# Kernel tuning notes

Measured on AMD Instinct MI355X. Metric: run time of the kernel, lower is better.

The kernel has to match this reference:

```python
import jax, jax.numpy as jnp
import numpy as np

K = 16          # neighboursnum
NEG_SLOPE = 0.01  # torch LeakyReLU default
EPS = 1e-5      # torch BatchNorm default


def _bn(x, gamma, beta, axes):
    # BatchNorm in training mode: biased batch stats over `axes`, channel dim = 1
    mu = x.mean(axes, keepdims=True)
    var = x.var(axes, keepdims=True)
    shape = [1] * x.ndim
    shape[1] = -1
    return (x - mu) / jnp.sqrt(var + EPS) * gamma.reshape(shape) + beta.reshape(shape)


def _lrelu(x):
    return jnp.where(x >= 0, x, NEG_SLOPE * x)


def setup_inputs() -> dict:
    key = jax.random.key(0)
    ks = jax.random.split(key, 9)
    B, D, N, O = 4, 64, 4096, 128
    s = 0.05
    return {
        "f_in": jax.random.normal(ks[0], (B, D, N), jnp.float32),
        "w_local": jax.random.normal(ks[1], (O, 2 * D + 1), jnp.float32) * s,
        "g_local": jnp.ones((O,), jnp.float32),
        "b_local": jnp.zeros((O,), jnp.float32),
        "w_sem": jax.random.normal(ks[2], (O, D), jnp.float32) * s,
        "g_sem": jnp.ones((O,), jnp.float32),
        "b_sem": jnp.zeros((O,), jnp.float32),
        "w_full": jax.random.normal(ks[3], (O, 2 * O), jnp.float32) * s,
        "g_full": jnp.ones((O,), jnp.float32),
        "b_full": jnp.zeros((O,), jnp.float32),
        "wq": jax.random.normal(ks[4], (D, D), jnp.float32) * s,
        "bq": jax.random.normal(ks[5], (D,), jnp.float32) * s,
        "wk": jax.random.normal(ks[6], (D, D), jnp.float32) * s,
        "bk": jax.random.normal(ks[7], (D,), jnp.float32) * s,
        "wv": jax.random.normal(ks[8], (D, D), jnp.float32) * s,
        "bv": jax.random.normal(jax.random.fold_in(key, 99), (D,), jnp.float32) * s,
    }


def reference(f_in, w_local, g_local, b_local, w_sem, g_sem, b_sem,
              w_full, g_full, b_full, wq, bq, wk, bk, wv, bv):
    B, D, N = f_in.shape
    # --- knn on feature space: pairwise negative squared distance, topk ---
    xx = jnp.sum(f_in * f_in, axis=1)                       # (B,N)
    inner = jnp.einsum('bdm,bdn->bmn', f_in, f_in)          # (B,N,N)
    pd = -xx[:, :, None] + 2.0 * inner - xx[:, None, :]     # -||xi-xj||^2
    idx = jax.lax.top_k(pd, K)[1]                           # (B,N,K) nearest
    # --- gather graph feature ---
    x_t = jnp.swapaxes(f_in, 1, 2)                          # (B,N,D)
    neigh = x_t[jnp.arange(B)[:, None, None], idx]          # (B,N,K,D)
    central = jnp.broadcast_to(x_t[:, :, None, :], neigh.shape)
    dist = jnp.linalg.norm(neigh - central, axis=3, keepdims=True)  # (B,N,K,1)
    feat = jnp.concatenate([central, neigh, dist], axis=3)  # (B,N,K,2D+1)
    feat = jnp.transpose(feat, (0, 3, 1, 2))                # (B,2D+1,N,K)
    # --- localConv (1x1 conv2d, no bias) + BN2d + LeakyReLU, max over K ---
    intra = _lrelu(_bn(jnp.einsum('oc,bcnk->bonk', w_local, feat),
                       g_local, b_local, (0, 2, 3)))
    intra = intra.max(axis=-1)                              # (B,O,N)
    # --- self-attention over points ---
    q = jnp.einsum('od,bdn->bon', wq, f_in) + bq[None, :, None]
    k = jnp.einsum('od,bdn->bon', wk, f_in) + bk[None, :, None]
    v = jnp.einsum('od,bdn->bon', wv, f_in) + bv[None, :, None]
    scores = jax.nn.softmax(
        jnp.einsum('bdm,bdn->bmn', q, k) / jnp.sqrt(jnp.float32(D)), axis=-1)
    fgt = jnp.einsum('bmn,bdn->bdm', scores, v)             # (B,D,N)
    # --- semConv (1x1 conv1d) + BN1d + LeakyReLU ---
    inter = _lrelu(_bn(jnp.einsum('od,bdn->bon', w_sem, fgt),
                       g_sem, b_sem, (0, 2)))               # (B,O,N)
    # --- fullConv on concat ---
    cat = jnp.concatenate([intra, inter], axis=1)           # (B,2O,N)
    out = _lrelu(_bn(jnp.einsum('oc,bcn->bon', w_full, cat),
                     g_full, b_full, (0, 2)))               # (B,O,N)
    return out
```

## Files before the change

### kernel.cpp

```cpp
#include <hip/hip_runtime.h>
#include <math.h>

constexpr int NB = 4;
constexpr int ND = 64;
constexpr int NNN = 4096;
constexpr int NO = 128;
constexpr int NK = 16;
constexpr float NEG = 0.01f;
constexpr float BN_EPS = 1e-5f;

typedef unsigned short u16;
typedef unsigned int u32;
typedef __attribute__((ext_vector_type(8))) short short8;
typedef __attribute__((ext_vector_type(4))) float floatx4;

constexpr int OFF_XX    = 0;
constexpr int OFF_IDX   = 16384;
constexpr int OFF_D2    = 278528;
constexpr int OFF_Q     = 540672;
constexpr int OFF_K     = 1589248;
constexpr int OFF_V     = 2637824;
constexpr int OFF_FGT   = 3686400;
constexpr int OFF_APRE  = 4734976;
constexpr int OFF_BPRE  = 6832128;
constexpr int OFF_IMAX  = 8929280;
constexpr int OFF_IMIN  = 11026432;
constexpr int OFF_ZSEM  = OFF_Q;
constexpr int OFF_ZFULL = OFF_V;
constexpr int OFF_STATS = 13123584;
constexpr int OFF_COEF  = 13124352;
constexpr int OFF_LINV  = 13125120;

__device__ __forceinline__ u16 f2b(float x) {
  u32 u = __builtin_bit_cast(u32, x);
  u += 0x7fffu + ((u >> 16) & 1u);
  return (u16)(u >> 16);
}
__device__ __forceinline__ float b2f(u16 h) {
  u32 u = (u32)h << 16;
  return __builtin_bit_cast(float, u);
}

template <int CTRL>
__device__ __forceinline__ float fmax_dpp(float v) {
  int b = __builtin_bit_cast(int, v);
  int s = __builtin_amdgcn_update_dpp(b, b, CTRL, 0xF, 0xF, false);
  return fmaxf(v, __builtin_bit_cast(float, s));
}
__device__ __forceinline__ void pairmax(float av, int ai, float bv, int bi, float& rv, int& ri) {
  bool tk = bv > av;
  rv = tk ? bv : av;
  ri = tk ? bi : ai;
}

__global__ void k_xx(const float* __restrict__ f, float* __restrict__ xx) {
  int gid = blockIdx.x * 256 + threadIdx.x;
  int b = gid >> 12, n = gid & 4095;
  const float* fb = f + b * ND * NNN + n;
  float s = 0.f;
#pragma unroll
  for (int d = 0; d < ND; ++d) { float v = fb[d * NNN]; s += v * v; }
  xx[gid] = s;
}

__global__ __launch_bounds__(256) void k_qkv(const float* __restrict__ f,
    const float* __restrict__ wq, const float* __restrict__ bq,
    const float* __restrict__ wk, const float* __restrict__ bk,
    const float* __restrict__ wv, const float* __restrict__ bv,
    u16* __restrict__ qb, u16* __restrict__ kb, u16* __restrict__ vb) {
  int sel = blockIdx.y;
  const float* W    = (sel == 0) ? wq : (sel == 1) ? wk : wv;
  const float* bias = (sel == 0) ? bq : (sel == 1) ? bk : bv;
  int t = threadIdx.x;
  int lane = t & 63;
  int og = __builtin_amdgcn_readfirstlane(t >> 6);
  int gcol = blockIdx.x * 64 + lane;
  int b = gcol >> 12, n = gcol & 4095;
  const float* fb = f + b * ND * NNN + n;
  float cv[64];
#pragma unroll
  for (int d = 0; d < ND; ++d) cv[d] = fb[d * NNN];
  float acc[16];
#pragma unroll 1
  for (int oi = 0; oi < 16; ++oi) {
    int o = og * 16 + oi;
    const float* wr = W + o * ND;
    float a = bias[o];
#pragma unroll
    for (int d = 0; d < ND; ++d) a += wr[d] * cv[d];
    acc[oi] = a;
  }
  if (sel == 2) {
#pragma unroll
    for (int oi = 0; oi < 16; ++oi)
      vb[(size_t)(b * ND + og * 16 + oi) * NNN + n] = f2b(acc[oi]);
  } else {
    short8 p0, p1;
#pragma unroll
    for (int oi = 0; oi < 8; ++oi) { p0[oi] = (short)f2b(acc[oi]); p1[oi] = (short)f2b(acc[8 + oi]); }
    u16* dst = (sel ? kb : qb) + (size_t)(b * NNN + n) * ND + og * 16;
    *(short8*)dst = p0;
    *(short8*)(dst + 8) = p1;
  }
}

__global__ __launch_bounds__(256, 4) void k_knn(const float* __restrict__ f, const float* __restrict__ xx,
                                                int* __restrict__ tidx, float* __restrict__ td2) {
  __shared__ __align__(16) float fm[ND * 8];
  __shared__ __align__(16) float sl[4 * 2048];
  int t = threadIdx.x;
  int lane = t & 63;
  int w = __builtin_amdgcn_readfirstlane(t >> 6);
  int b = blockIdx.x >> 9;
  int m0 = (blockIdx.x & 511) << 3;
  const float* fb = f + b * ND * NNN;
  { int e = t;       int d = e >> 3, r = e & 7; fm[e] = fb[d * NNN + m0 + r]; }
  { int e = t + 256; int d = e >> 3, r = e & 7; fm[e] = fb[d * NNN + m0 + r]; }
  __syncthreads();
  float lv[2][2];
  int   li[2][2];
#pragma unroll
  for (int h = 0; h < 2; ++h) {
    float acc[64];
#pragma unroll
    for (int i = 0; i < 64; ++i) acc[i] = 0.f;
    for (int d = 0; d < ND; ++d) {
      const float* frow = fb + d * NNN + h * 2048 + 4 * t;
      float4 v0 = *(const float4*)(frow);
      float4 v1 = *(const float4*)(frow + 1024);
      float4 r0 = *(const float4*)&fm[d * 8];
      float4 r1 = *(const float4*)&fm[d * 8 + 4];
      float va0[4] = {v0.x, v0.y, v0.z, v0.w};
      float va1[4] = {v1.x, v1.y, v1.z, v1.w};
      float rr[8]  = {r0.x, r0.y, r0.z, r0.w, r1.x, r1.y, r1.z, r1.w};
#pragma unroll
      for (int c2 = 0; c2 < 4; ++c2)
#pragma unroll
        for (int r = 0; r < 8; ++r) {
          acc[c2 * 8 + r]      += va0[c2] * rr[r];
          acc[32 + c2 * 8 + r] += va1[c2] * rr[r];
        }
    }
    {
      const float* xrow = xx + b * NNN + h * 2048 + 4 * t;
      float4 x0 = *(const float4*)(xrow);
      float4 x1 = *(const float4*)(xrow + 1024);
      float xa0[4] = {x0.x, x0.y, x0.z, x0.w};
      float xa1[4] = {x1.x, x1.y, x1.z, x1.w};
#pragma unroll
      for (int c2 = 0; c2 < 4; ++c2)
#pragma unroll
        for (int r = 0; r < 8; ++r) {
          acc[c2 * 8 + r]      = 2.f * acc[c2 * 8 + r]      - xa0[c2];
          acc[32 + c2 * 8 + r] = 2.f * acc[32 + c2 * 8 + r] - xa1[c2];
        }
    }
#pragma unroll
    for (int s = 0; s < 2; ++s) {
      __syncthreads();
#pragma unroll
      for (int r4 = 0; r4 < 4; ++r4) {
        int r = s * 4 + r4;
#pragma unroll
        for (int jj = 0; jj < 2; ++jj) {
          float4 w4;
          w4.x = acc[jj * 32 + 0 * 8 + r];
          w4.y = acc[jj * 32 + 1 * 8 + r];
          w4.z = acc[jj * 32 + 2 * 8 + r];
          w4.w = acc[jj * 32 + 3 * 8 + r];
          *(float4*)&sl[r4 * 2048 + jj * 1024 + 4 * t] = w4;
        }
      }
      __syncthreads();
      float vals[32];
#pragma unroll
      for (int i = 0; i < 32; ++i) vals[i] = sl[w * 2048 + i * 64 + lane];
      float gv[8]; int gi[8];
#pragma unroll
      for (int g = 0; g < 8; ++g) {
        float v0 = vals[g * 4]; int i0 = (g * 4) * 64 + lane;
#pragma unroll
        for (int k2 = 1; k2 < 4; ++k2)
          pairmax(v0, i0, vals[g * 4 + k2], (g * 4 + k2) * 64 + lane, v0, i0);
        gv[g] = v0; gi[g] = i0;
      }
      float t1v[4]; int t1i[4];
      float t2v[2]; int t2i[2];
      float lvv; int lii;
#pragma unroll
      for (int p = 0; p < 4; ++p) pairmax(gv[2 * p], gi[2 * p], gv[2 * p + 1], gi[2 * p + 1], t1v[p], t1i[p]);
#pragma unroll
      for (int q = 0; q < 2; ++q) pairmax(t1v[2 * q], t1i[2 * q], t1v[2 * q + 1], t1i[2 * q + 1], t2v[q], t2i[q]);
      pairmax(t2v[0], t2i[0], t2v[1], t2i[1], lvv, lii);
      float selv = 0.f; int seli = 0;
#pragma unroll 1
      for (int kx = 0; kx < NK; ++kx) {
        float W = lvv;
        W = fmax_dpp<0xB1>(W);
        W = fmax_dpp<0x4E>(W);
        W = fmax_dpp<0x124>(W);
        W = fmax_dpp<0x128>(W);
        W = fmaxf(W, __shfl_xor(W, 16));
        W = fmaxf(W, __shfl_xor(W, 32));
        unsigned long long mk = __ballot(lvv == W);
        int lw = (int)__ffsll(mk) - 1;
        int wcol = __builtin_amdgcn_readlane(lii, lw);
        if (lane == kx) { selv = W; seli = wcol; }
        int jw = wcol >> 6;
#pragma unroll
        for (int g = 0; g < 8; ++g)
          if (g == (jw >> 2)) {
#pragma unroll
            for (int k2 = 0; k2 < 4; ++k2)
              if (k2 == (jw & 3))
                vals[g * 4 + k2] = (lane == lw) ? -3.0e38f : vals[g * 4 + k2];
            float v0 = vals[g * 4]; int i0 = (g * 4) * 64 + lane;
#pragma unroll
            for (int k2 = 1; k2 < 4; ++k2)
              pairmax(v0, i0, vals[g * 4 + k2], (g * 4 + k2) * 64 + lane, v0, i0);
            gv[g] = v0; gi[g] = i0;
            int p = g >> 1;
            pairmax(gv[2 * p], gi[2 * p], gv[2 * p + 1], gi[2 * p + 1], t1v[p], t1i[p]);
            int q = p >> 1;
            pairmax(t1v[2 * q], t1i[2 * q], t1v[2 * q + 1], t1i[2 * q + 1], t2v[q], t2i[q]);
            pairmax(t2v[0], t2i[0], t2v[1], t2i[1], lvv, lii);
          }
      }
      lv[h][s] = selv; li[h][s] = h * 2048 + seli;
    }
  }
#pragma unroll
  for (int s = 0; s < 2; ++s) {
    int m = m0 + s * 4 + w;
    float xm = xx[b * NNN + m];
    float a   = lv[0][s]; int ai  = li[0][s];
    float bb2 = lv[1][s]; int bi2 = li[1][s];
    int cntB = 0, cntA = 0;
#pragma unroll
    for (int j = 0; j < 16; ++j) {
      float bj = __shfl(bb2, j);
      cntB += (bj > a) ? 1 : 0;
      float aj = __shfl(a, j);
      cntA += (aj >= bb2) ? 1 : 0;
    }
    if (lane < 16) {
      int base = (b * NNN + m) * NK;
      int rA = lane + cntB;
      int rB = lane + cntA;
      if (rA < NK) {
        float dd = xm - a;
        tidx[base + rA] = ai;
        td2[base + rA] = dd > 0.f ? dd : 0.f;
      }
      if (rB < NK) {
        float dd = xm - bb2;
        tidx[base + rB] = bi2;
        td2[base + rB] = dd > 0.f ? dd : 0.f;
      }
    }
  }
}

__global__ __launch_bounds__(256) void k_attn(const u16* __restrict__ qb,
                                              const u16* __restrict__ kb,
                                              const u16* __restrict__ vb,
                                              float* __restrict__ fgt,
                                              float* __restrict__ linv) {
  __shared__ __align__(16) u16 P[32 * 520];
  __shared__ float rsum[4][32];
  int t = threadIdx.x;
  int lane = t & 63;
  int w = __builtin_amdgcn_readfirstlane(t >> 6);
  int quad = lane >> 4;
  int l15 = lane & 15;
  int b = blockIdx.x >> 7;
  int m0 = (blockIdx.x & 127) << 5;
  const u16* qra = qb + (size_t)(b * NNN + m0 + l15) * ND + quad * 8;
  const u16* qrb = qb + (size_t)(b * NNN + m0 + 16 + l15) * ND + quad * 8;
  short8 qa0a = *(const short8*)(qra), qa1a = *(const short8*)(qra + 32);
  short8 qa0b = *(const short8*)(qrb), qa1b = *(const short8*)(qrb + 32);
  const u16* kbase = kb + (size_t)b * NNN * ND;
  const u16* vrow  = vb + (size_t)(b * ND + w * 16 + l15) * NNN;
  floatx4 c2a = {0.f, 0.f, 0.f, 0.f};
  floatx4 c2b = {0.f, 0.f, 0.f, 0.f};
  float rsa[4] = {0.f, 0.f, 0.f, 0.f};
  float rsb[4] = {0.f, 0.f, 0.f, 0.f};
#pragma unroll 1
  for (int it = 0; it < 8; ++it) {
    int nchunk = it * 512;
#pragma unroll 1
    for (int ct = 0; ct < 8; ++ct) {
      int cc0 = (w * 8 + ct) * 16;
      const u16* krow = kbase + (size_t)(nchunk + cc0 + l15) * ND + quad * 8;
      short8 kf0 = *(const short8*)(krow);
      short8 kf1 = *(const short8*)(krow + 32);
      floatx4 acca = {0.f, 0.f, 0.f, 0.f};
      acca = __builtin_amdgcn_mfma_f32_16x16x32_bf16(qa0a, kf0, acca, 0, 0, 0);
      acca = __builtin_amdgcn_mfma_f32_16x16x32_bf16(qa1a, kf1, acca, 0, 0, 0);
      floatx4 accb = {0.f, 0.f, 0.f, 0.f};
      accb = __builtin_amdgcn_mfma_f32_16x16x32_bf16(qa0b, kf0, accb, 0, 0, 0);
      accb = __builtin_amdgcn_mfma_f32_16x16x32_bf16(qa1b, kf1, accb, 0, 0, 0);
      int ccol = cc0 + l15;
#pragma unroll
      for (int r = 0; r < 4; ++r) {
        float ea = __expf(acca[r] * 0.125f);
        rsa[r] += ea;
        P[(quad * 4 + r) * 520 + ccol] = f2b(ea);
        float eb = __expf(accb[r] * 0.125f);
        rsb[r] += eb;
        P[(16 + quad * 4 + r) * 520 + ccol] = f2b(eb);
      }
    }
    __syncthreads();
    const u16* vp = vrow + nchunk + quad * 8;
#pragma unroll
    for (int kk = 0; kk < 16; ++kk) {
      short8 b2 = *(const short8*)(vp + kk * 32);
      short8 a2a = *(const short8*)&P[l15 * 520 + kk * 32 + quad * 8];
      short8 a2b = *(const short8*)&P[(16 + l15) * 520 + kk * 32 + quad * 8];
      c2a = __builtin_amdgcn_mfma_f32_16x16x32_bf16(a2a, b2, c2a, 0, 0, 0);
      c2b = __builtin_amdgcn_mfma_f32_16x16x32_bf16(a2b, b2, c2b, 0, 0, 0);
    }
    __syncthreads();
  }
#pragma unroll
  for (int r = 0; r < 4; ++r) {
    float va = rsa[r];
    va += __shfl_xor(va, 1); va += __shfl_xor(va, 2);
    va += __shfl_xor(va, 4); va += __shfl_xor(va, 8);
    rsa[r] = va;
    float vb2 = rsb[r];
    vb2 += __shfl_xor(vb2, 1); vb2 += __shfl_xor(vb2, 2);
    vb2 += __shfl_xor(vb2, 4); vb2 += __shfl_xor(vb2, 8);
    rsb[r] = vb2;
  }
  if (l15 == 0) {
#pragma unroll
    for (int r = 0; r < 4; ++r) {
      rsum[w][quad * 4 + r] = rsa[r];
      rsum[w][16 + quad * 4 + r] = rsb[r];
    }
  }
#pragma unroll
  for (int r = 0; r < 4; ++r) {
    fgt[(size_t)(b * NNN + m0 + quad * 4 + r) * ND + w * 16 + l15] = c2a[r];
    fgt[(size_t)(b * NNN + m0 + 16 + quad * 4 + r) * ND + w * 16 + l15] = c2b[r];
  }
  __syncthreads();
  if (t < 32) {
    float s = rsum[0][t] + rsum[1][t] + rsum[2][t] + rsum[3][t];
    linv[b * NNN + m0 + t] = 1.f / s;
  }
}

__global__ __launch_bounds__(256) void k_ab(const float* __restrict__ f, const float* __restrict__ wl,
                                            u16* __restrict__ Apre, u16* __restrict__ Bpre) {
  __shared__ float fl[ND * 64];
  int t = threadIdx.x;
  int b = blockIdx.x >> 6;
  int n0 = (blockIdx.x & 63) << 6;
  for (int e = t; e < ND * 64; e += 256) {
    int d = e >> 6, c = e & 63;
    fl[e] = f[b * ND * NNN + d * NNN + n0 + c];
  }
  __syncthreads();
  int lane = t & 63;
  int w = __builtin_amdgcn_readfirstlane(t >> 6);
#pragma unroll 1
  for (int g = 0; g < 8; ++g) {
    float acc[8] = {0, 0, 0, 0, 0, 0, 0, 0};
    int p0 = w * 64 + g * 8;
    for (int d = 0; d < ND; ++d) {
      float fv = fl[d * 64 + lane];
#pragma unroll
      for (int u = 0; u < 8; ++u) {
        int p = p0 + u;
        int o = p & 127, sel = p >> 7;
        acc[u] += wl[o * 129 + sel * 64 + d] * fv;
      }
    }
#pragma unroll
    for (int u = 0; u < 8; ++u) {
      int p = p0 + u;
      int o = p & 127, sel = p >> 7;
      u16* outp = sel ? Bpre : Apre;
      outp[(size_t)(b * NNN + n0 + lane) * NO + o] = f2b(acc[u]);
    }
  }
}

__global__ __launch_bounds__(128) void k_intra(const u16* __restrict__ Apre, const u16* __restrict__ Bpre,
                                               const int* __restrict__ tidx, const float* __restrict__ td2,
                                               const float* __restrict__ wl, float* __restrict__ imax,
                                               float* __restrict__ imin, float* __restrict__ stats) {
  __shared__ int sidx[32 * NK];
  __shared__ float sdst[32 * NK];
  int t = threadIdx.x;
  int b = blockIdx.x >> 7;
  int n0 = (blockIdx.x & 127) << 5;
  for (int e = t; e < 32 * NK; e += 128) {
    int base = (b * NNN + n0 + (e >> 4)) * NK + (e & 15);
    sidx[e] = tidx[base];
    sdst[e] = sqrtf(td2[base]);
  }
  __syncthreads();
  int o = t;
  float w128 = wl[o * 129 + 128];
  float ssum = 0.f, ssq = 0.f;
  for (int c = 0; c < 32; ++c) {
    float a = b2f(Apre[(size_t)(b * NNN + n0 + c) * NO + o]);
    float mx = -3.4e38f, mn = 3.4e38f;
#pragma unroll
    for (int kx = 0; kx < NK; ++kx) {
      int id = sidx[c * NK + kx];
      float y = a + b2f(Bpre[(size_t)(b * NNN + id) * NO + o]) + w128 * sdst[c * NK + kx];
      mx = fmaxf(mx, y); mn = fminf(mn, y);
      ssum += y; ssq += y * y;
    }
    imax[(b * NO + o) * NNN + n0 + c] = mx;
    imin[(b * NO + o) * NNN + n0 + c] = mn;
  }
  atomicAdd(&stats[o], ssum);
  atomicAdd(&stats[NO + o], ssq);
}

__global__ __launch_bounds__(256) void k_sem(const float* __restrict__ fgt, const float* __restrict__ linv,
                                             const float* __restrict__ wsem, float* __restrict__ zsem) {
  __shared__ float fl[64 * 65];
  int t = threadIdx.x;
  int b = blockIdx.x >> 6;
  int n0 = (blockIdx.x & 63) << 6;
  for (int e = t; e < 64 * 64; e += 256) {
    int n = e >> 6, d = e & 63;
    fl[n * 65 + d] = fgt[(size_t)(b * NNN + n0 + n) * ND + d] * linv[b * NNN + n0 + n];
  }
  __syncthreads();
  int lane = t & 63;
  int ob = __builtin_amdgcn_readfirstlane((t >> 6) * 32);
#pragma unroll 1
  for (int g = 0; g < 4; ++g) {
    float acc[8] = {0, 0, 0, 0, 0, 0, 0, 0};
    for (int d = 0; d < ND; ++d) {
      float fv = fl[lane * 65 + d];
#pragma unroll
      for (int u = 0; u < 8; ++u) acc[u] += wsem[(ob + g * 8 + u) * ND + d] * fv;
    }
#pragma unroll
    for (int u = 0; u < 8; ++u)
      zsem[(b * NO + ob + g * 8 + u) * NNN + n0 + lane] = acc[u];
  }
}

__global__ void k_stats(const float* __restrict__ zz, float* __restrict__ sout) {
  int o = blockIdx.x, t = threadIdx.x;
  float s = 0.f, q = 0.f;
  for (int b2 = 0; b2 < NB; ++b2) {
    const float* p = zz + (size_t)(b2 * NO + o) * NNN;
    for (int n = t; n < NNN; n += 256) { float v = p[n]; s += v; q += v * v; }
  }
#pragma unroll
  for (int off = 32; off; off >>= 1) { s += __shfl_down(s, off); q += __shfl_down(q, off); }
  __shared__ float rs[4], rq[4];
  int lane = t & 63, w = t >> 6;
  if (lane == 0) { rs[w] = s; rq[w] = q; }
  __syncthreads();
  if (t == 0) {
    sout[o]      = rs[0] + rs[1] + rs[2] + rs[3];
    sout[NO + o] = rq[0] + rq[1] + rq[2] + rq[3];
  }
}

__global__ void k_fin2(const float* __restrict__ stats,
                       const float* __restrict__ g1, const float* __restrict__ be1, float ci1,
                       const float* __restrict__ g2, const float* __restrict__ be2, float ci2,
                       float* __restrict__ coef) {
  int t = threadIdx.x;
  int o = t & 127;
  int which = t >> 7;
  const float* st = stats + which * 2 * NO;
  const float* g  = which ? g2 : g1;
  const float* be = which ? be2 : be1;
  float ci = which ? ci2 : ci1;
  float mean = st[o] * ci;
  float var = st[NO + o] * ci - mean * mean;
  var = var > 0.f ? var : 0.f;
  float a = g[o] * rsqrtf(var + BN_EPS);
  coef[which * 2 * NO + o] = a;
  coef[which * 2 * NO + NO + o] = be[o] - mean * a;
}

__global__ void k_fin(const float* __restrict__ stats, const float* __restrict__ g,
                      const float* __restrict__ be, float cnt_inv, float* __restrict__ coef) {
  int o = threadIdx.x;
  float mean = stats[o] * cnt_inv;
  float var = stats[NO + o] * cnt_inv - mean * mean;
  var = var > 0.f ? var : 0.f;
  float a = g[o] * rsqrtf(var + BN_EPS);
  coef[o] = a;
  coef[NO + o] = be[o] - mean * a;
}

__global__ __launch_bounds__(256) void k_full(const float* __restrict__ imax, const float* __restrict__ imin,
                                              const float* __restrict__ zsem, const float* __restrict__ wfull,
                                              const float* __restrict__ coef, float* __restrict__ zfull) {
  __shared__ float fl[2 * NO * 64];
  int t = threadIdx.x;
  int b = blockIdx.x >> 6;
  int n0 = (blockIdx.x & 63) << 6;
  for (int e = t; e < 2 * NO * 64; e += 256) {
    int c = e >> 6, col = e & 63;
    float aa, bb, x;
    if (c < NO) {
      aa = coef[c]; bb = coef[NO + c];
      const float* src = (aa >= 0.f) ? imax : imin;
      x = src[(b * NO + c) * NNN + n0 + col];
    } else {
      int c2 = c - NO;
      aa = coef[2 * NO + c2]; bb = coef[3 * NO + c2];
      x = zsem[(b * NO + c2) * NNN + n0 + col];
    }
    float y = aa * x + bb;
    fl[e] = (y >= 0.f) ? y : NEG * y;
  }
  __syncthreads();
  int lane = t & 63;
  int ob = __builtin_amdgcn_readfirstlane((t >> 6) * 32);
#pragma unroll 1
  for (int g = 0; g < 4; ++g) {
    float acc[8] = {0, 0, 0, 0, 0, 0, 0, 0};
    for (int c = 0; c < 2 * NO; ++c) {
      float fv = fl[c * 64 + lane];
#pragma unroll
      for (int u = 0; u < 8; ++u) acc[u] += wfull[(ob + g * 8 + u) * (2 * NO) + c] * fv;
    }
#pragma unroll
    for (int u = 0; u < 8; ++u)
      zfull[(b * NO + ob + g * 8 + u) * NNN + n0 + lane] = acc[u];
  }
}

__global__ void k_out(const float* __restrict__ zfull, const float* __restrict__ coef,
                      float* __restrict__ out) {
  int gid = blockIdx.x * 256 + threadIdx.x;
  int o = (gid >> 12) & 127;
  float y = coef[o] * zfull[gid] + coef[NO + o];
  out[gid] = (y >= 0.f) ? y : NEG * y;
}

extern "C" void kernel_launch(void* const* d_in, const int* in_sizes, int n_in,
                              void* d_out, int out_size, void* d_ws, size_t ws_size,
                              hipStream_t stream) {
  (void)in_sizes; (void)n_in; (void)out_size; (void)ws_size;
  const float* f       = (const float*)d_in[0];
  const float* w_local = (const float*)d_in[1];
  const float* g_local = (const float*)d_in[2];
  const float* b_local = (const float*)d_in[3];
  const float* w_sem   = (const float*)d_in[4];
  const float* g_sem   = (const float*)d_in[5];
  const float* b_sem   = (const float*)d_in[6];
  const float* w_full  = (const float*)d_in[7];
  const float* g_full  = (const float*)d_in[8];
  const float* b_full  = (const float*)d_in[9];
  const float* wq = (const float*)d_in[10];
  const float* bq = (const float*)d_in[11];
  const float* wk = (const float*)d_in[12];
  const float* bk = (const float*)d_in[13];
  const float* wv = (const float*)d_in[14];
  const float* bv = (const float*)d_in[15];
  float* Wp = (float*)d_ws;
  u16* qb16 = (u16*)(Wp + OFF_Q);
  u16* kb16 = (u16*)(Wp + OFF_K);
  u16* vb16 = (u16*)(Wp + OFF_V);
  u16* ap16 = (u16*)(Wp + OFF_APRE);
  u16* bp16 = (u16*)(Wp + OFF_BPRE);

  hipMemsetAsync(Wp + OFF_STATS, 0, 2 * NO * sizeof(float), stream);
  k_xx  <<<NB * NNN / 256, 256, 0, stream>>>(f, Wp + OFF_XX);
  k_qkv <<<dim3(NB * NNN / 64, 3), 256, 0, stream>>>(f, wq, bq, wk, bk, wv, bv, qb16, kb16, vb16);
  k_knn <<<NB * (NNN / 8), 256, 0, stream>>>(f, Wp + OFF_XX, (int*)(Wp + OFF_IDX), Wp + OFF_D2);
  k_attn<<<NB * (NNN / 32), 256, 0, stream>>>(qb16, kb16, vb16, Wp + OFF_FGT, Wp + OFF_LINV);
  k_ab  <<<NB * (NNN / 64), 256, 0, stream>>>(f, w_local, ap16, bp16);
  k_intra<<<NB * (NNN / 32), 128, 0, stream>>>(ap16, bp16,
                                               (const int*)(Wp + OFF_IDX), Wp + OFF_D2,
                                               w_local, Wp + OFF_IMAX, Wp + OFF_IMIN, Wp + OFF_STATS);
  k_sem <<<NB * (NNN / 64), 256, 0, stream>>>(Wp + OFF_FGT, Wp + OFF_LINV, w_sem, Wp + OFF_ZSEM);
  k_stats<<<NO, 256, 0, stream>>>(Wp + OFF_ZSEM, Wp + OFF_STATS + 2 * NO);
  k_fin2<<<1, 2 * NO, 0, stream>>>(Wp + OFF_STATS,
                                   g_local, b_local, 1.f / (float)(NB * NNN * NK),
                                   g_sem, b_sem, 1.f / (float)(NB * NNN),
                                   Wp + OFF_COEF);
  k_full<<<NB * (NNN / 64), 256, 0, stream>>>(Wp + OFF_IMAX, Wp + OFF_IMIN, Wp + OFF_ZSEM,
                                              w_full, Wp + OFF_COEF, Wp + OFF_ZFULL);
  k_stats<<<NO, 256, 0, stream>>>(Wp + OFF_ZFULL, Wp + OFF_STATS + 4 * NO);
  k_fin <<<1, NO, 0, stream>>>(Wp + OFF_STATS + 4 * NO, g_full, b_full,
                               1.f / (float)(NB * NNN), Wp + OFF_COEF + 4 * NO);
  k_out <<<NB * NO * NNN / 256, 256, 0, stream>>>(Wp + OFF_ZFULL, Wp + OFF_COEF + 4 * NO,
                                                  (float*)d_out);
}
```

Baseline: 632.2 us.

## Fold xx into qkv, split intra rows, parallelize stats, drop fin kernel

Computes the squared norms inside k_qkv from registers it already holds, which removes the separate k_xx launch. k_intra now runs 256 threads that split the 32 points between two halves, reduces the partial sums in shared memory and then issues the atomics. k_stats launches one block per (channel, batch) and accumulates with atomics, so the stats buffer is zeroed by a wider memset. The final BN coefficient step moves into k_out, which drops the k_fin launch but makes every output element redo the per-channel rsqrt.

```diff
diff --git a/kernel.cpp b/kernel.cpp
--- a/kernel.cpp
+++ b/kernel.cpp
@@ -53,21 +53,12 @@
   ri = tk ? bi : ai;
 }
 
-__global__ void k_xx(const float* __restrict__ f, float* __restrict__ xx) {
-  int gid = blockIdx.x * 256 + threadIdx.x;
-  int b = gid >> 12, n = gid & 4095;
-  const float* fb = f + b * ND * NNN + n;
-  float s = 0.f;
-#pragma unroll
-  for (int d = 0; d < ND; ++d) { float v = fb[d * NNN]; s += v * v; }
-  xx[gid] = s;
-}
-
 __global__ __launch_bounds__(256) void k_qkv(const float* __restrict__ f,
     const float* __restrict__ wq, const float* __restrict__ bq,
     const float* __restrict__ wk, const float* __restrict__ bk,
     const float* __restrict__ wv, const float* __restrict__ bv,
-    u16* __restrict__ qb, u16* __restrict__ kb, u16* __restrict__ vb) {
+    u16* __restrict__ qb, u16* __restrict__ kb, u16* __restrict__ vb,
+    float* __restrict__ xx) {
   int sel = blockIdx.y;
   const float* W    = (sel == 0) ? wq : (sel == 1) ? wk : wv;
   const float* bias = (sel == 0) ? bq : (sel == 1) ? bk : bv;
@@ -80,6 +71,12 @@
   float cv[64];
 #pragma unroll
   for (int d = 0; d < ND; ++d) cv[d] = fb[d * NNN];
+  if (sel == 0 && og == 0) {
+    float s = 0.f;
+#pragma unroll
+    for (int d = 0; d < ND; ++d) s += cv[d] * cv[d];
+    xx[b * NNN + n] = s;
+  }
   float acc[16];
 #pragma unroll 1
   for (int oi = 0; oi < 16; ++oi) {
@@ -389,25 +386,27 @@
   }
 }
 
-__global__ __launch_bounds__(128) void k_intra(const u16* __restrict__ Apre, const u16* __restrict__ Bpre,
+__global__ __launch_bounds__(256) void k_intra(const u16* __restrict__ Apre, const u16* __restrict__ Bpre,
                                                const int* __restrict__ tidx, const float* __restrict__ td2,
                                                const float* __restrict__ wl, float* __restrict__ imax,
                                                float* __restrict__ imin, float* __restrict__ stats) {
   __shared__ int sidx[32 * NK];
   __shared__ float sdst[32 * NK];
+  __shared__ float ps[128], pq[128];
   int t = threadIdx.x;
   int b = blockIdx.x >> 7;
   int n0 = (blockIdx.x & 127) << 5;
-  for (int e = t; e < 32 * NK; e += 128) {
+  for (int e = t; e < 32 * NK; e += 256) {
     int base = (b * NNN + n0 + (e >> 4)) * NK + (e & 15);
     sidx[e] = tidx[base];
     sdst[e] = sqrtf(td2[base]);
   }
   __syncthreads();
-  int o = t;
+  int o = t & 127;
+  int ch = t >> 7;
   float w128 = wl[o * 129 + 128];
   float ssum = 0.f, ssq = 0.f;
-  for (int c = 0; c < 32; ++c) {
+  for (int c = ch * 16; c < ch * 16 + 16; ++c) {
     float a = b2f(Apre[(size_t)(b * NNN + n0 + c) * NO + o]);
     float mx = -3.4e38f, mn = 3.4e38f;
 #pragma unroll
@@ -420,8 +419,12 @@
     imax[(b * NO + o) * NNN + n0 + c] = mx;
     imin[(b * NO + o) * NNN + n0 + c] = mn;
   }
-  atomicAdd(&stats[o], ssum);
-  atomicAdd(&stats[NO + o], ssq);
+  if (t >= 128) { ps[o] = ssum; pq[o] = ssq; }
+  __syncthreads();
+  if (t < 128) {
+    atomicAdd(&stats[o], ssum + ps[o]);
+    atomicAdd(&stats[NO + o], ssq + pq[o]);
+  }
 }
 
 __global__ __launch_bounds__(256) void k_sem(const float* __restrict__ fgt, const float* __restrict__ linv,
@@ -452,12 +455,10 @@
 }
 
 __global__ void k_stats(const float* __restrict__ zz, float* __restrict__ sout) {
-  int o = blockIdx.x, t = threadIdx.x;
+  int o = blockIdx.x, b2 = blockIdx.y, t = threadIdx.x;
+  const float* p = zz + (size_t)(b2 * NO + o) * NNN;
   float s = 0.f, q = 0.f;
-  for (int b2 = 0; b2 < NB; ++b2) {
-    const float* p = zz + (size_t)(b2 * NO + o) * NNN;
-    for (int n = t; n < NNN; n += 256) { float v = p[n]; s += v; q += v * v; }
-  }
+  for (int n = t; n < NNN; n += 256) { float v = p[n]; s += v; q += v * v; }
 #pragma unroll
   for (int off = 32; off; off >>= 1) { s += __shfl_down(s, off); q += __shfl_down(q, off); }
   __shared__ float rs[4], rq[4];
@@ -465,8 +466,8 @@
   if (lane == 0) { rs[w] = s; rq[w] = q; }
   __syncthreads();
   if (t == 0) {
-    sout[o]      = rs[0] + rs[1] + rs[2] + rs[3];
-    sout[NO + o] = rq[0] + rq[1] + rq[2] + rq[3];
+    atomicAdd(&sout[o],      rs[0] + rs[1] + rs[2] + rs[3]);
+    atomicAdd(&sout[NO + o], rq[0] + rq[1] + rq[2] + rq[3]);
   }
 }
 
@@ -487,17 +488,6 @@
   float a = g[o] * rsqrtf(var + BN_EPS);
   coef[which * 2 * NO + o] = a;
   coef[which * 2 * NO + NO + o] = be[o] - mean * a;
-}
-
-__global__ void k_fin(const float* __restrict__ stats, const float* __restrict__ g,
-                      const float* __restrict__ be, float cnt_inv, float* __restrict__ coef) {
-  int o = threadIdx.x;
-  float mean = stats[o] * cnt_inv;
-  float var = stats[NO + o] * cnt_inv - mean * mean;
-  var = var > 0.f ? var : 0.f;
-  float a = g[o] * rsqrtf(var + BN_EPS);
-  coef[o] = a;
-  coef[NO + o] = be[o] - mean * a;
 }
 
 __global__ __launch_bounds__(256) void k_full(const float* __restrict__ imax, const float* __restrict__ imin,
@@ -539,11 +529,17 @@
   }
 }
 
-__global__ void k_out(const float* __restrict__ zfull, const float* __restrict__ coef,
+__global__ void k_out(const float* __restrict__ zfull, const float* __restrict__ stats,
+                      const float* __restrict__ g, const float* __restrict__ be, float ci,
                       float* __restrict__ out) {
   int gid = blockIdx.x * 256 + threadIdx.x;
   int o = (gid >> 12) & 127;
-  float y = coef[o] * zfull[gid] + coef[NO + o];
+  float mean = stats[o] * ci;
+  float var = stats[NO + o] * ci - mean * mean;
+  var = var > 0.f ? var : 0.f;
+  float a = g[o] * rsqrtf(var + BN_EPS);
+  float bb = be[o] - mean * a;
+  float y = a * zfull[gid] + bb;
   out[gid] = (y >= 0.f) ? y : NEG * y;
 }
 
@@ -574,26 +570,25 @@
   u16* ap16 = (u16*)(Wp + OFF_APRE);
   u16* bp16 = (u16*)(Wp + OFF_BPRE);
 
-  hipMemsetAsync(Wp + OFF_STATS, 0, 2 * NO * sizeof(float), stream);
-  k_xx  <<<NB * NNN / 256, 256, 0, stream>>>(f, Wp + OFF_XX);
-  k_qkv <<<dim3(NB * NNN / 64, 3), 256, 0, stream>>>(f, wq, bq, wk, bk, wv, bv, qb16, kb16, vb16);
+  hipMemsetAsync(Wp + OFF_STATS, 0, 6 * NO * sizeof(float), stream);
+  k_qkv <<<dim3(NB * NNN / 64, 3), 256, 0, stream>>>(f, wq, bq, wk, bk, wv, bv,
+                                                     qb16, kb16, vb16, Wp + OFF_XX);
   k_knn <<<NB * (NNN / 8), 256, 0, stream>>>(f, Wp + OFF_XX, (int*)(Wp + OFF_IDX), Wp + OFF_D2);
   k_attn<<<NB * (NNN / 32), 256, 0, stream>>>(qb16, kb16, vb16, Wp + OFF_FGT, Wp + OFF_LINV);
   k_ab  <<<NB * (NNN / 64), 256, 0, stream>>>(f, w_local, ap16, bp16);
-  k_intra<<<NB * (NNN / 32), 128, 0, stream>>>(ap16, bp16,
+  k_intra<<<NB * (NNN / 32), 256, 0, stream>>>(ap16, bp16,
                                                (const int*)(Wp + OFF_IDX), Wp + OFF_D2,
                                                w_local, Wp + OFF_IMAX, Wp + OFF_IMIN, Wp + OFF_STATS);
   k_sem <<<NB * (NNN / 64), 256, 0, stream>>>(Wp + OFF_FGT, Wp + OFF_LINV, w_sem, Wp + OFF_ZSEM);
-  k_stats<<<NO, 256, 0, stream>>>(Wp + OFF_ZSEM, Wp + OFF_STATS + 2 * NO);
+  k_stats<<<dim3(NO, NB), 256, 0, stream>>>(Wp + OFF_ZSEM, Wp + OFF_STATS + 2 * NO);
   k_fin2<<<1, 2 * NO, 0, stream>>>(Wp + OFF_STATS,
                                    g_local, b_local, 1.f / (float)(NB * NNN * NK),
                                    g_sem, b_sem, 1.f / (float)(NB * NNN),
                                    Wp + OFF_COEF);
   k_full<<<NB * (NNN / 64), 256, 0, stream>>>(Wp + OFF_IMAX, Wp + OFF_IMIN, Wp + OFF_ZSEM,
                                               w_full, Wp + OFF_COEF, Wp + OFF_ZFULL);
-  k_stats<<<NO, 256, 0, stream>>>(Wp + OFF_ZFULL, Wp + OFF_STATS + 4 * NO);
-  k_fin <<<1, NO, 0, stream>>>(Wp + OFF_STATS + 4 * NO, g_full, b_full,
-                               1.f / (float)(NB * NNN), Wp + OFF_COEF + 4 * NO);
-  k_out <<<NB * NO * NNN / 256, 256, 0, stream>>>(Wp + OFF_ZFULL, Wp + OFF_COEF + 4 * NO,
+  k_stats<<<dim3(NO, NB), 256, 0, stream>>>(Wp + OFF_ZFULL, Wp + OFF_STATS + 4 * NO);
+  k_out <<<NB * NO * NNN / 256, 256, 0, stream>>>(Wp + OFF_ZFULL, Wp + OFF_STATS + 4 * NO,
+                                                  g_full, b_full, 1.f / (float)(NB * NNN),
                                                   (float*)d_out);
 }
```

New measurement: 597.4 us. 5.5% less time.
